# Kernel optimization log

Measured on AMD Instinct MI355X. Metric: run time of the kernel, lower is better.

The kernel has to match this reference:

```python
import jax, jax.numpy as jnp
import numpy as np

N_NODES = 8192
N_EDGES = 65536
D_MODEL = 64
D_INNER = 128
D_STATE = 16
DT_RANK = 4
LAYER_NUM = 3
TAU = 0.01


def _unif(key, shape, fan_out):
    stdv = 1.0 / np.sqrt(fan_out)
    return jax.random.uniform(key, shape, jnp.float32, -stdv, stdv)


def setup_inputs() -> dict:
    key = jax.random.key(0)
    ks = jax.random.split(key, 12)
    x = jax.random.normal(ks[0], (N_NODES, D_MODEL), jnp.float32)
    edge_index = jax.random.randint(ks[1], (2, N_EDGES), 0, N_NODES, jnp.int64)
    in_proj_w = _unif(ks[2], (D_MODEL, 2 * D_INNER), 2 * D_INNER)
    x_proj_w = _unif(ks[3], (D_INNER, DT_RANK + 2 * D_STATE), DT_RANK + 2 * D_STATE)
    dt_proj_w = _unif(ks[4], (DT_RANK, D_INNER), D_INNER)
    out_proj_w = _unif(ks[5], (D_INNER, D_MODEL), D_MODEL)
    A_log = jnp.log(jnp.broadcast_to(jnp.arange(1, D_STATE + 1, dtype=jnp.float32)[None, :], (D_INNER, D_STATE)))
    D = jnp.ones((D_INNER,), jnp.float32)
    in_act_w = _unif(ks[6], (D_INNER, 2), 2)
    in_act_b = _unif(ks[7], (2,), 2)
    out_act_w = _unif(ks[8], (D_INNER, 2), 2)
    out_act_b = _unif(ks[9], (2,), 2)
    return {"x": x, "in_proj_w": in_proj_w, "x_proj_w": x_proj_w, "dt_proj_w": dt_proj_w,
            "A_log": A_log, "D": D, "out_proj_w": out_proj_w,
            "in_act_w": in_act_w, "in_act_b": in_act_b, "out_act_w": out_act_w, "out_act_b": out_act_b,
            "edge_index": edge_index, "layer_num": LAYER_NUM}


def _norm_adj(row, col, w, n_nodes):
    # SparseTensor(...).set_diag() adds diag value 1; symmetric deg^-1/2 renorm
    deg = jax.ops.segment_sum(w, row, num_segments=n_nodes) + 1.0
    dinv = jnp.where(deg > 0, deg ** -0.5, 0.0)
    return dinv[row] * w * dinv[col], dinv * dinv  # off-diag edge weights, diag weights


def _spmm(row, col, ew, dw, x, n_nodes):
    # adj @ x with adj = edges(ew) + diag(dw); x: [N, F]
    return jax.ops.segment_sum(ew[:, None] * x[col], row, num_segments=n_nodes) + dw[:, None] * x


def _gumbel_hard(logits, key, tau):
    g = jax.random.gumbel(key, logits.shape, logits.dtype)
    y = jax.nn.softmax((logits + g) / tau, axis=-1)
    hard = jax.nn.one_hot(jnp.argmax(y, axis=-1), logits.shape[-1], dtype=y.dtype)
    return hard + y - jax.lax.stop_gradient(y)


def reference(x, in_proj_w, x_proj_w, dt_proj_w, A_log, D, out_proj_w,
              in_act_w, in_act_b, out_act_w, out_act_b, edge_index, layer_num):
    n_nodes, d_model = x.shape
    d_inner = dt_proj_w.shape[1]
    n = A_log.shape[1]
    dt_rank = dt_proj_w.shape[0]
    row, col = edge_index[0], edge_index[1]

    xl = jnp.broadcast_to(x[:, None, :], (n_nodes, layer_num, d_model))  # [N,L,d_model]
    x_and_res = xl @ in_proj_w                                           # [N,L,2*d_inner]
    xs, res = jnp.split(x_and_res, 2, axis=-1)
    xs = jax.nn.relu(xs)                                                 # u in scan

    A = -jnp.exp(A_log)                                                  # [d_inner, n]
    x_dbl = xs @ x_proj_w                                                # [N,L,dt_rank+2n]
    delta = jax.nn.softplus(x_dbl[..., :dt_rank] @ dt_proj_w)            # [N,L,d_inner]
    B = x_dbl[..., dt_rank:dt_rank + n]                                  # [N,L,n]
    C = x_dbl[..., dt_rank + n:]                                         # [N,L,n]

    deltaA = jnp.exp(jnp.einsum('bld,dn->bldn', delta, A))               # [N,L,d_inner,n]
    deltaB_u = jnp.einsum('bld,bln->bldn', delta * xs, B)                # [N,L,d_inner,n]

    # initial adjacency: unit-weight edges, sym-normalized with self loops
    ew, dw = _norm_adj(row, col, jnp.ones((row.shape[0],), xs.dtype), n_nodes)
    state = jnp.zeros((n_nodes, d_inner, n), xs.dtype)
    gkey = jax.random.key(42)
    ys = []
    for i in range(layer_num):  # small fixed number of GCN/SSM steps
        state = deltaA[:, i] * state + deltaB_u[:, i]
        y = jnp.einsum('bdn,bn->bd', state, C[:, i])                     # [N,d_inner]
        flat = _spmm(row, col, ew, dw, state.reshape(n_nodes, d_inner * n), n_nodes)
        state = flat.reshape(n_nodes, d_inner, n)
        in_p = _gumbel_hard(y @ in_act_w + in_act_b, jax.random.fold_in(gkey, 2 * i), TAU)
        out_p = _gumbel_hard(y @ out_act_w + out_act_b, jax.random.fold_in(gkey, 2 * i + 1), TAU)
        w = in_p[col, 0] * out_p[row, 0]  # keep_in_prob[v] * keep_out_prob[u]
        ew, dw = _norm_adj(row, col, w, n_nodes)
        ys.append(y)

    y = jnp.stack(ys, axis=1) + xs * D                                   # [N,L,d_inner]
    y = y * jax.nn.relu(res)
    out = y @ out_proj_w                                                 # [N,L,d_model]
    return out[:, -1, :]
```

## Files before the change

### kernel.cpp

```cpp
#include <hip/hip_runtime.h>
#include <cstdint>

#define NN 8192
#define NE 65536
#define G 8
#define CAP 64

typedef _Float16 h8 __attribute__((ext_vector_type(8)));
typedef _Float16 h2 __attribute__((ext_vector_type(2)));

__host__ __device__ inline void tf2x32(uint32_t k0, uint32_t k1,
                                       uint32_t x0, uint32_t x1,
                                       uint32_t& r0, uint32_t& r1) {
  uint32_t ks2 = k0 ^ k1 ^ 0x1BD11BDAu;
  x0 += k0; x1 += k1;
#define TF_ROT(x,d) (((x)<<(d))|((x)>>(32-(d))))
#define TF_R4(ra,rb,rc,rd) \
  x0+=x1; x1=TF_ROT(x1,ra); x1^=x0; \
  x0+=x1; x1=TF_ROT(x1,rb); x1^=x0; \
  x0+=x1; x1=TF_ROT(x1,rc); x1^=x0; \
  x0+=x1; x1=TF_ROT(x1,rd); x1^=x0;
  TF_R4(13,15,26,6)  x0+=k1;  x1+=ks2+1u;
  TF_R4(17,29,16,24) x0+=ks2; x1+=k0+2u;
  TF_R4(13,15,26,6)  x0+=k0;  x1+=k1+3u;
  TF_R4(17,29,16,24) x0+=k1;  x1+=ks2+4u;
  TF_R4(13,15,26,6)  x0+=ks2; x1+=k0+5u;
  r0=x0; r1=x1;
#undef TF_R4
#undef TF_ROT
}

__device__ inline float gumbel32(uint32_t k0, uint32_t k1, uint32_t idx) {
  uint32_t a, b;
  tf2x32(k0, k1, 0u, idx, a, b);
  uint32_t bits = a ^ b;
  float f = __uint_as_float((bits >> 9) | 0x3f800000u) - 1.0f;
  float u = (f > 0.0f) ? f : 1.17549435e-38f;
  return -logf(-logf(u));
}

__global__ void k_scatter(const int* __restrict__ ei, int* __restrict__ cnt,
                          int* __restrict__ csr_col) {
  int e = blockIdx.x*blockDim.x + threadIdx.x;
  if (e < NE) {
    int v = ei[e];
    int pos = atomicAdd(&cnt[v], 1);
    if (pos < CAP) csr_col[(v<<6) + pos] = ei[NE + e];
  }
}

__global__ __launch_bounds__(256) void k_nodeprep(
    const float* __restrict__ x, const float* __restrict__ ipw,
    const float* __restrict__ xpw, const float* __restrict__ dtw,
    const float* __restrict__ iaw, const float* __restrict__ iab,
    const float* __restrict__ oaw, const float* __restrict__ oab,
    const float* __restrict__ alog,
    uint32_t ki0, uint32_t ki1, uint32_t ko0, uint32_t ko1,
    float* __restrict__ xs, float* __restrict__ rres,
    float* __restrict__ delta, _Float16* __restrict__ dxh2,
    float* __restrict__ Bm, _Float16* __restrict__ Bh,
    float* __restrict__ Cm,
    float* __restrict__ inp, float* __restrict__ outp,
    float* __restrict__ Amat) {
  __shared__ float sx[G][64];
  __shared__ float sxs[G][128];
  __shared__ float sdbl[G][36];
  __shared__ float sdx[G][128];
  int t = threadIdx.x;
  int b0 = blockIdx.x * G;
  if (blockIdx.x == 0) {
    for (int i = t; i < 2048; i += 256) Amat[i] = -expf(alog[i]);
  }
  for (int i = t; i < G*64; i += 256) sx[i>>6][i&63] = x[b0*64 + i];
  __syncthreads();
  float acc[G];
#pragma unroll
  for (int g = 0; g < G; g++) acc[g] = 0.f;
  for (int k = 0; k < 64; k++) {
    float w = ipw[k*256 + t];
#pragma unroll
    for (int g = 0; g < G; g++) acc[g] += sx[g][k] * w;
  }
  if (t < 128) {
#pragma unroll
    for (int g = 0; g < G; g++) {
      float v = fmaxf(acc[g], 0.f);
      sxs[g][t] = v;
      xs[(size_t)(b0+g)*128 + t] = v;
    }
  } else {
    int j = t - 128;
#pragma unroll
    for (int g = 0; g < G; g++) rres[(size_t)(b0+g)*128 + j] = fmaxf(acc[g], 0.f);
  }
  __syncthreads();
  for (int idx = t; idx < G*36; idx += 256) {
    int g = idx / 36, c = idx % 36;
    float a = 0.f;
    for (int d = 0; d < 128; d++) a += sxs[g][d] * xpw[d*36 + c];
    sdbl[g][c] = a;
    if (c >= 4 && c < 20) {
      Bm[(b0+g)*16 + (c-4)] = a;
      Bh[(b0+g)*16 + (c-4)] = (_Float16)a;
    } else if (c >= 20)    Cm[(b0+g)*16 + (c-20)] = a;
  }
  __syncthreads();
  {
    int d = t & 127, hi = t >> 7;
#pragma unroll
    for (int gg = 0; gg < G/2; gg++) {
      int g = hi*(G/2) + gg;
      int b = b0 + g;
      float dt = sdbl[g][0]*dtw[d]     + sdbl[g][1]*dtw[128+d]
               + sdbl[g][2]*dtw[256+d] + sdbl[g][3]*dtw[384+d];
      float dv = fmaxf(dt, 0.f) + log1pf(expf(-fabsf(dt)));
      delta[(size_t)b*128 + d] = dv;
      sdx[g][d] = dv * sxs[g][d];
    }
  }
  __syncthreads();
  for (int i = t; i < G*64; i += 256) {
    int g = i >> 6, d = i & 63;
    h2 pk;
    pk.x = (_Float16)sdx[g][d];
    pk.y = (_Float16)sdx[g][d + 64];
    ((h2*)(dxh2 + ((size_t)(b0+g) << 7)))[d] = pk;
  }
  int wid = t >> 6, lane = t & 63;
#pragma unroll
  for (int s = 0; s < 2; s++) {
    int g = wid*2 + s;
    int b = b0 + g;
    float da = sdx[g][lane], db = sdx[g][lane + 64];
    float4 pr;
    pr.x = da*iaw[2*lane]   + db*iaw[2*(lane+64)];
    pr.y = da*iaw[2*lane+1] + db*iaw[2*(lane+64)+1];
    pr.z = da*oaw[2*lane]   + db*oaw[2*(lane+64)];
    pr.w = da*oaw[2*lane+1] + db*oaw[2*(lane+64)+1];
    for (int off = 32; off >= 1; off >>= 1) {
      pr.x += __shfl_down(pr.x, off);
      pr.y += __shfl_down(pr.y, off);
      pr.z += __shfl_down(pr.z, off);
      pr.w += __shfl_down(pr.w, off);
    }
    if (lane == 0) {
      float BC = 0.f;
      for (int n = 0; n < 16; n++) BC += sdbl[g][4+n] * sdbl[g][20+n];
      float li0 = BC*pr.x + iab[0], li1 = BC*pr.y + iab[1];
      float lo0 = BC*pr.z + oab[0], lo1 = BC*pr.w + oab[1];
      uint32_t L0 = 2u*(uint32_t)b, L1 = L0 + 1u;
      inp[b]  = (li0 + gumbel32(ki0, ki1, L0) >= li1 + gumbel32(ki0, ki1, L1)) ? 1.0f : 0.0f;
      outp[b] = (lo0 + gumbel32(ko0, ko1, L0) >= lo1 + gumbel32(ko0, ko1, L1)) ? 1.0f : 0.0f;
    }
  }
}

__global__ __launch_bounds__(256) void k_spmm0f(
    const int* __restrict__ cnt, const int* __restrict__ csr_col,
    const float* __restrict__ inp, const float* __restrict__ outp,
    const float* __restrict__ delta, const _Float16* __restrict__ dxh2,
    const float* __restrict__ Bm, const _Float16* __restrict__ Bh,
    const float* __restrict__ Cm, const float* __restrict__ Amat,
    _Float16* __restrict__ s_out, float* __restrict__ dinv1,
    float* __restrict__ y2p) {
  __shared__ int   sc[2][CAP];
  __shared__ float scoef[2][CAP];
  __shared__ float sdegs[2];
  int t = threadIdx.x, half = t >> 7, tid2 = t & 127;
  int v = (blockIdx.x << 1) + half;
  int deg = min(cnt[v], CAP);
  if (tid2 < 64) {
    float g = 0.f;
    if (tid2 < deg) {
      int c = csr_col[(v<<6) + tid2];
      sc[half][tid2] = c;
      scoef[half][tid2] = 1.0f / sqrtf((float)min(cnt[c], CAP) + 1.0f);
      g = inp[c];
    }
    for (int off = 32; off >= 1; off >>= 1) g += __shfl_down(g, off);
    if (tid2 == 0) sdegs[half] = g;
  }
  __syncthreads();
  int d0 = tid2 >> 1, d1 = d0 + 64, nq = tid2 & 1;
  float dv = 1.0f / sqrtf((float)deg + 1.0f);
  const float4* BmV = (const float4*)(Bm + ((size_t)v << 4));
  float4 Bv0 = BmV[nq*2], Bv1 = BmV[nq*2+1];
  h2 pkv = ((const h2*)(dxh2 + ((size_t)v << 7)))[d0];
  float dx0 = (float)pkv.x, dx1 = (float)pkv.y;
  float dw = dv * dv;
  float c0 = dw * dx0, c1 = dw * dx1;
  float4 a0l = {c0*Bv0.x, c0*Bv0.y, c0*Bv0.z, c0*Bv0.w};
  float4 a0h = {c0*Bv1.x, c0*Bv1.y, c0*Bv1.z, c0*Bv1.w};
  float4 a1l = {c1*Bv0.x, c1*Bv0.y, c1*Bv0.z, c1*Bv0.w};
  float4 a1h = {c1*Bv1.x, c1*Bv1.y, c1*Bv1.z, c1*Bv1.w};
  for (int j = 0; j < deg; j++) {
    int c = sc[half][j];
    float coef = dv * scoef[half][j];
    h2 pk = ((const h2*)(dxh2 + ((size_t)c << 7)))[d0];
    h8 Bp = ((const h8*)(Bh + ((size_t)c << 4)))[nq];
    float e0 = coef * (float)pk.x;
    float e1 = coef * (float)pk.y;
    float b0f = (float)Bp[0], b1f = (float)Bp[1], b2f = (float)Bp[2], b3f = (float)Bp[3];
    float b4f = (float)Bp[4], b5f = (float)Bp[5], b6f = (float)Bp[6], b7f = (float)Bp[7];
    a0l.x += e0*b0f; a0l.y += e0*b1f; a0l.z += e0*b2f; a0l.w += e0*b3f;
    a0h.x += e0*b4f; a0h.y += e0*b5f; a0h.z += e0*b6f; a0h.w += e0*b7f;
    a1l.x += e1*b0f; a1l.y += e1*b1f; a1l.z += e1*b2f; a1l.w += e1*b3f;
    a1h.x += e1*b4f; a1h.y += e1*b5f; a1h.z += e1*b6f; a1h.w += e1*b7f;
  }
  float de0 = delta[v*128 + d0], de1 = delta[v*128 + d1];
  const float4* A0p = (const float4*)(Amat + (d0 << 4));
  const float4* A1p = (const float4*)(Amat + (d1 << 4));
  float4 A00 = A0p[nq*2], A01 = A0p[nq*2+1];
  float4 A10 = A1p[nq*2], A11 = A1p[nq*2+1];
  float4 E0l, E0h, E1l, E1h;
  E0l.x = expf(de0*A00.x); E0l.y = expf(de0*A00.y); E0l.z = expf(de0*A00.z); E0l.w = expf(de0*A00.w);
  E0h.x = expf(de0*A01.x); E0h.y = expf(de0*A01.y); E0h.z = expf(de0*A01.z); E0h.w = expf(de0*A01.w);
  E1l.x = expf(de1*A10.x); E1l.y = expf(de1*A10.y); E1l.z = expf(de1*A10.z); E1l.w = expf(de1*A10.w);
  E1h.x = expf(de1*A11.x); E1h.y = expf(de1*A11.y); E1h.z = expf(de1*A11.z); E1h.w = expf(de1*A11.w);
  float4 s0l, s0h, s1l, s1h;
  s0l.x = E0l.x*a0l.x + dx0*Bv0.x; s0l.y = E0l.y*a0l.y + dx0*Bv0.y;
  s0l.z = E0l.z*a0l.z + dx0*Bv0.z; s0l.w = E0l.w*a0l.w + dx0*Bv0.w;
  s0h.x = E0h.x*a0h.x + dx0*Bv1.x; s0h.y = E0h.y*a0h.y + dx0*Bv1.y;
  s0h.z = E0h.z*a0h.z + dx0*Bv1.z; s0h.w = E0h.w*a0h.w + dx0*Bv1.w;
  s1l.x = E1l.x*a1l.x + dx1*Bv0.x; s1l.y = E1l.y*a1l.y + dx1*Bv0.y;
  s1l.z = E1l.z*a1l.z + dx1*Bv0.z; s1l.w = E1l.w*a1l.w + dx1*Bv0.w;
  s1h.x = E1h.x*a1h.x + dx1*Bv1.x; s1h.y = E1h.y*a1h.y + dx1*Bv1.y;
  s1h.z = E1h.z*a1h.z + dx1*Bv1.z; s1h.w = E1h.w*a1h.w + dx1*Bv1.w;
  if (inp[v] != 0.f) {
    h8* op = (h8*)(s_out + ((size_t)v << 11));
    h8 p0, p1;
    p0[0]=(_Float16)s0l.x; p0[1]=(_Float16)s0l.y; p0[2]=(_Float16)s0l.z; p0[3]=(_Float16)s0l.w;
    p0[4]=(_Float16)s0h.x; p0[5]=(_Float16)s0h.y; p0[6]=(_Float16)s0h.z; p0[7]=(_Float16)s0h.w;
    p1[0]=(_Float16)s1l.x; p1[1]=(_Float16)s1l.y; p1[2]=(_Float16)s1l.z; p1[3]=(_Float16)s1l.w;
    p1[4]=(_Float16)s1h.x; p1[5]=(_Float16)s1h.y; p1[6]=(_Float16)s1h.z; p1[7]=(_Float16)s1h.w;
    op[d0*2 + nq] = p0;
    op[d0*2 + 128 + nq] = p1;
  }
  float degs = sdegs[half];
  float d1v = 1.0f / sqrtf(outp[v]*degs + 1.0f);
  if (tid2 == 0) dinv1[v] = d1v;
  float dw1 = d1v * d1v;
  const float4* CmV = (const float4*)(Cm + ((size_t)v << 4));
  float4 Cv0 = CmV[nq*2], Cv1 = CmV[nq*2+1];
  float BvC = Bv0.x*Cv0.x + Bv0.y*Cv0.y + Bv0.z*Cv0.z + Bv0.w*Cv0.w
            + Bv1.x*Cv1.x + Bv1.y*Cv1.y + Bv1.z*Cv1.z + Bv1.w*Cv1.w;
  float y0p = dw1*(E0l.x*s0l.x*Cv0.x + E0l.y*s0l.y*Cv0.y + E0l.z*s0l.z*Cv0.z + E0l.w*s0l.w*Cv0.w
                 + E0h.x*s0h.x*Cv1.x + E0h.y*s0h.y*Cv1.y + E0h.z*s0h.z*Cv1.z + E0h.w*s0h.w*Cv1.w)
            + dx0*BvC;
  float y1p = dw1*(E1l.x*s1l.x*Cv0.x + E1l.y*s1l.y*Cv0.y + E1l.z*s1l.z*Cv0.z + E1l.w*s1l.w*Cv0.w
                 + E1h.x*s1h.x*Cv1.x + E1h.y*s1h.y*Cv1.y + E1h.z*s1h.z*Cv1.z + E1h.w*s1h.w*Cv1.w)
            + dx1*BvC;
  y0p += __shfl_xor(y0p, 1);
  y1p += __shfl_xor(y1p, 1);
  if (nq == 0) {
    y2p[v*128 + d0] = y0p;
    y2p[v*128 + d1] = y1p;
  }
}

__global__ __launch_bounds__(256) void k_spmm1fo(
    const int* __restrict__ cnt, const int* __restrict__ csr_col,
    const float* __restrict__ dinv1,
    const float* __restrict__ inp, const float* __restrict__ outp,
    const float* __restrict__ delta,
    const float* __restrict__ Cm, const float* __restrict__ Amat,
    const _Float16* __restrict__ s_in, const float* __restrict__ y2p,
    const float* __restrict__ xs, const float* __restrict__ rres,
    const float* __restrict__ Dv, const float* __restrict__ wout,
    float* __restrict__ out) {
  __shared__ int   sc[2][CAP];
  __shared__ float scoef[2][CAP];
  __shared__ int   snact[2];
  __shared__ float ty[2][128];
  __shared__ float sproj[2][64];
  int t = threadIdx.x, half = t >> 7, tid2 = t & 127;
  int v = (blockIdx.x << 1) + half;
  if (tid2 == 0) snact[half] = 0;
  if (tid2 < 64) {
    int deg = (outp[v] != 0.f) ? min(cnt[v], CAP) : 0;
    if (tid2 < deg) {
      int c = csr_col[(v<<6) + tid2];
      if (inp[c] != 0.f) {
        int p = atomicAdd(&snact[half], 1);
        sc[half][p] = c; scoef[half][p] = dinv1[c];
      }
    }
  }
  __syncthreads();
  int nact = snact[half];
  int d0 = tid2 >> 1, d1 = d0 + 64, nq = tid2 & 1;
  float dv = dinv1[v];
  float4 a0l = {0.f,0.f,0.f,0.f}, a0h = {0.f,0.f,0.f,0.f};
  float4 a1l = {0.f,0.f,0.f,0.f}, a1h = {0.f,0.f,0.f,0.f};
  for (int j = 0; j < nact; j++) {
    int c = sc[half][j];
    float coef = dv * scoef[half][j];
    const h8* rp = (const h8*)(s_in + ((size_t)c << 11));
    h8 n0 = rp[d0*2 + nq], n1 = rp[d0*2 + 128 + nq];
    a0l.x += coef*(float)n0[0]; a0l.y += coef*(float)n0[1];
    a0l.z += coef*(float)n0[2]; a0l.w += coef*(float)n0[3];
    a0h.x += coef*(float)n0[4]; a0h.y += coef*(float)n0[5];
    a0h.z += coef*(float)n0[6]; a0h.w += coef*(float)n0[7];
    a1l.x += coef*(float)n1[0]; a1l.y += coef*(float)n1[1];
    a1l.z += coef*(float)n1[2]; a1l.w += coef*(float)n1[3];
    a1h.x += coef*(float)n1[4]; a1h.y += coef*(float)n1[5];
    a1h.z += coef*(float)n1[6]; a1h.w += coef*(float)n1[7];
  }
  float y0g = 0.f, y1g = 0.f;
  if (nact > 0) {
    float de0 = delta[v*128 + d0], de1 = delta[v*128 + d1];
    const float4* A0p = (const float4*)(Amat + (d0 << 4));
    const float4* A1p = (const float4*)(Amat + (d1 << 4));
    float4 A00 = A0p[nq*2], A01 = A0p[nq*2+1];
    float4 A10 = A1p[nq*2], A11 = A1p[nq*2+1];
    const float4* CmV = (const float4*)(Cm + ((size_t)v << 4));
    float4 Cv0 = CmV[nq*2], Cv1 = CmV[nq*2+1];
    y0g = expf(de0*A00.x)*a0l.x*Cv0.x + expf(de0*A00.y)*a0l.y*Cv0.y
        + expf(de0*A00.z)*a0l.z*Cv0.z + expf(de0*A00.w)*a0l.w*Cv0.w
        + expf(de0*A01.x)*a0h.x*Cv1.x + expf(de0*A01.y)*a0h.y*Cv1.y
        + expf(de0*A01.z)*a0h.z*Cv1.z + expf(de0*A01.w)*a0h.w*Cv1.w;
    y1g = expf(de1*A10.x)*a1l.x*Cv0.x + expf(de1*A10.y)*a1l.y*Cv0.y
        + expf(de1*A10.z)*a1l.z*Cv0.z + expf(de1*A10.w)*a1l.w*Cv0.w
        + expf(de1*A11.x)*a1h.x*Cv1.x + expf(de1*A11.y)*a1h.y*Cv1.y
        + expf(de1*A11.z)*a1h.z*Cv1.z + expf(de1*A11.w)*a1h.w*Cv1.w;
  }
  y0g += __shfl_xor(y0g, 1);
  y1g += __shfl_xor(y1g, 1);
  if (nq == 0) {
    float yA = y0g + y2p[v*128 + d0];
    float yB = y1g + y2p[v*128 + d1];
    ty[half][d0] = (yA + xs[v*128 + d0]*Dv[d0]) * rres[v*128 + d0];
    ty[half][d1] = (yB + xs[v*128 + d1]*Dv[d1]) * rres[v*128 + d1];
  }
  __syncthreads();
  int oc = tid2 & 63, ks = tid2 >> 6;
  const float* typ = ty[half];
  float acc = 0.f;
  for (int d = ks*64; d < ks*64 + 64; d++) acc += typ[d] * wout[d*64 + oc];
  if (ks == 1) sproj[half][oc] = acc;
  __syncthreads();
  if (ks == 0) out[v*64 + oc] = acc + sproj[half][oc];
}

extern "C" void kernel_launch(void* const* d_in, const int* in_sizes, int n_in,
                              void* d_out, int out_size, void* d_ws, size_t ws_size,
                              hipStream_t stream) {
  const float* x    = (const float*)d_in[0];
  const float* ipw  = (const float*)d_in[1];
  const float* xpw  = (const float*)d_in[2];
  const float* dtw  = (const float*)d_in[3];
  const float* alog = (const float*)d_in[4];
  const float* Dv   = (const float*)d_in[5];
  const float* wout = (const float*)d_in[6];
  const float* iaw  = (const float*)d_in[7];
  const float* iab  = (const float*)d_in[8];
  const float* oaw  = (const float*)d_in[9];
  const float* oab  = (const float*)d_in[10];
  const int*   ei   = (const int*)d_in[11];
  (void)in_sizes; (void)n_in; (void)out_size; (void)ws_size;

  float* W = (float*)d_ws;
  size_t o = 0;
  float* xs    = W + o; o += (size_t)NN*128;
  float* rres  = W + o; o += (size_t)NN*128;
  float* delta = W + o; o += (size_t)NN*128;
  float* y2p   = W + o; o += (size_t)NN*128;
  float* Bm    = W + o; o += (size_t)NN*16;
  float* Cm    = W + o; o += (size_t)NN*16;
  float* Amat  = W + o; o += 2048;
  float* dinv1 = W + o; o += NN;
  float* inp   = W + o; o += NN;
  float* outp  = W + o; o += NN;
  _Float16* dxh2 = (_Float16*)(W + o); o += (size_t)NN*64;
  _Float16* Bh   = (_Float16*)(W + o); o += (size_t)NN*8;
  _Float16* stA  = (_Float16*)(W + o); o += (size_t)NN*1024;
  int* cnt     = (int*)(W + o);
  int* csr_col = cnt + NN;

  uint32_t ki0, ki1, ko0, ko1;
  tf2x32(0u, 42u, 0u, 0u, ki0, ki1);
  tf2x32(0u, 42u, 0u, 1u, ko0, ko1);

  hipMemsetAsync(cnt, 0, NN*sizeof(int), stream);
  k_scatter<<<NE/256, 256, 0, stream>>>(ei, cnt, csr_col);

  k_nodeprep<<<NN/G, 256, 0, stream>>>(x, ipw, xpw, dtw, iaw, iab, oaw, oab,
                                       alog, ki0, ki1, ko0, ko1,
                                       xs, rres, delta, dxh2, Bm, Bh, Cm,
                                       inp, outp, Amat);

  k_spmm0f<<<NN/2, 256, 0, stream>>>(cnt, csr_col, inp, outp,
                                     delta, dxh2, Bm, Bh, Cm, Amat,
                                     stA, dinv1, y2p);

  k_spmm1fo<<<NN/2, 256, 0, stream>>>(cnt, csr_col, dinv1, inp, outp,
                                      delta, Cm, Amat, stA, y2p,
                                      xs, rres, Dv, wout, (float*)d_out);
}
```

Baseline: 168.8 us.

## Fuse edge scatter into nodeprep, stage fp16 out_proj in LDS, unroll gathers

Removes the separate CSR scatter kernel and folds the edge bucketing into k_nodeprep, where 64 threads per block handle one edge each (1024 blocks cover the 65536 edges). That kernel also converts out_proj weights to fp16. The final kernel copies those weights into 16KB of shared memory per block, so the output projection reads LDS instead of global memory. The neighbor-gather loops in both spmm kernels are unrolled by 4. This saves a launch and global weight reads, but costs fp16 precision in the output projection and per-block LDS copying that may lower occupancy.

```diff
diff --git a/kernel.cpp b/kernel.cpp
--- a/kernel.cpp
+++ b/kernel.cpp
@@ -39,35 +39,37 @@
   return -logf(-logf(u));
 }
 
-__global__ void k_scatter(const int* __restrict__ ei, int* __restrict__ cnt,
-                          int* __restrict__ csr_col) {
-  int e = blockIdx.x*blockDim.x + threadIdx.x;
-  if (e < NE) {
-    int v = ei[e];
-    int pos = atomicAdd(&cnt[v], 1);
-    if (pos < CAP) csr_col[(v<<6) + pos] = ei[NE + e];
-  }
-}
-
 __global__ __launch_bounds__(256) void k_nodeprep(
     const float* __restrict__ x, const float* __restrict__ ipw,
     const float* __restrict__ xpw, const float* __restrict__ dtw,
     const float* __restrict__ iaw, const float* __restrict__ iab,
     const float* __restrict__ oaw, const float* __restrict__ oab,
-    const float* __restrict__ alog,
+    const float* __restrict__ alog, const float* __restrict__ wout,
+    const int* __restrict__ ei,
     uint32_t ki0, uint32_t ki1, uint32_t ko0, uint32_t ko1,
     float* __restrict__ xs, float* __restrict__ rres,
     float* __restrict__ delta, _Float16* __restrict__ dxh2,
     float* __restrict__ Bm, _Float16* __restrict__ Bh,
     float* __restrict__ Cm,
     float* __restrict__ inp, float* __restrict__ outp,
-    float* __restrict__ Amat) {
+    float* __restrict__ Amat, _Float16* __restrict__ woh,
+    int* __restrict__ cnt, int* __restrict__ csr_col) {
   __shared__ float sx[G][64];
   __shared__ float sxs[G][128];
   __shared__ float sdbl[G][36];
   __shared__ float sdx[G][128];
   int t = threadIdx.x;
   int b0 = blockIdx.x * G;
+  if (t < 64) {
+    int e = blockIdx.x * 64 + t;
+    int v = ei[e];
+    int pos = atomicAdd(&cnt[v], 1);
+    if (pos < CAP) csr_col[(v<<6) + pos] = ei[NE + e];
+  }
+  {
+    int i = blockIdx.x * 8 + (t & 7);
+    if (t < 8) woh[i] = (_Float16)wout[i];
+  }
   if (blockIdx.x == 0) {
     for (int i = t; i < 2048; i += 256) Amat[i] = -expf(alog[i]);
   }
@@ -193,6 +195,7 @@
   float4 a0h = {c0*Bv1.x, c0*Bv1.y, c0*Bv1.z, c0*Bv1.w};
   float4 a1l = {c1*Bv0.x, c1*Bv0.y, c1*Bv0.z, c1*Bv0.w};
   float4 a1h = {c1*Bv1.x, c1*Bv1.y, c1*Bv1.z, c1*Bv1.w};
+#pragma unroll 4
   for (int j = 0; j < deg; j++) {
     int c = sc[half][j];
     float coef = dv * scoef[half][j];
@@ -266,15 +269,21 @@
     const float* __restrict__ Cm, const float* __restrict__ Amat,
     const _Float16* __restrict__ s_in, const float* __restrict__ y2p,
     const float* __restrict__ xs, const float* __restrict__ rres,
-    const float* __restrict__ Dv, const float* __restrict__ wout,
+    const float* __restrict__ Dv, const _Float16* __restrict__ woh,
     float* __restrict__ out) {
   __shared__ int   sc[2][CAP];
   __shared__ float scoef[2][CAP];
   __shared__ int   snact[2];
   __shared__ float ty[2][128];
   __shared__ float sproj[2][64];
+  __shared__ _Float16 swout[8192];
   int t = threadIdx.x, half = t >> 7, tid2 = t & 127;
   int v = (blockIdx.x << 1) + half;
+  {
+    const uint4* src = (const uint4*)woh;
+    uint4* dst = (uint4*)swout;
+    for (int i = t; i < 1024; i += 256) dst[i] = src[i];
+  }
   if (tid2 == 0) snact[half] = 0;
   if (tid2 < 64) {
     int deg = (outp[v] != 0.f) ? min(cnt[v], CAP) : 0;
@@ -292,6 +301,7 @@
   float dv = dinv1[v];
   float4 a0l = {0.f,0.f,0.f,0.f}, a0h = {0.f,0.f,0.f,0.f};
   float4 a1l = {0.f,0.f,0.f,0.f}, a1h = {0.f,0.f,0.f,0.f};
+#pragma unroll 4
   for (int j = 0; j < nact; j++) {
     int c = sc[half][j];
     float coef = dv * scoef[half][j];
@@ -336,7 +346,7 @@
   int oc = tid2 & 63, ks = tid2 >> 6;
   const float* typ = ty[half];
   float acc = 0.f;
-  for (int d = ks*64; d < ks*64 + 64; d++) acc += typ[d] * wout[d*64 + oc];
+  for (int d = ks*64; d < ks*64 + 64; d++) acc += typ[d] * (float)swout[d*64 + oc];
   if (ks == 1) sproj[half][oc] = acc;
   __syncthreads();
   if (ks == 0) out[v*64 + oc] = acc + sproj[half][oc];
@@ -373,6 +383,7 @@
   float* outp  = W + o; o += NN;
   _Float16* dxh2 = (_Float16*)(W + o); o += (size_t)NN*64;
   _Float16* Bh   = (_Float16*)(W + o); o += (size_t)NN*8;
+  _Float16* woh  = (_Float16*)(W + o); o += 4096;
   _Float16* stA  = (_Float16*)(W + o); o += (size_t)NN*1024;
   int* cnt     = (int*)(W + o);
   int* csr_col = cnt + NN;
@@ -382,12 +393,11 @@
   tf2x32(0u, 42u, 0u, 1u, ko0, ko1);
 
   hipMemsetAsync(cnt, 0, NN*sizeof(int), stream);
-  k_scatter<<<NE/256, 256, 0, stream>>>(ei, cnt, csr_col);
 
   k_nodeprep<<<NN/G, 256, 0, stream>>>(x, ipw, xpw, dtw, iaw, iab, oaw, oab,
-                                       alog, ki0, ki1, ko0, ko1,
+                                       alog, wout, ei, ki0, ki1, ko0, ko1,
                                        xs, rres, delta, dxh2, Bm, Bh, Cm,
-                                       inp, outp, Amat);
+                                       inp, outp, Amat, woh, cnt, csr_col);
 
   k_spmm0f<<<NN/2, 256, 0, stream>>>(cnt, csr_col, inp, outp,
                                      delta, dxh2, Bm, Bh, Cm, Amat,
@@ -395,5 +405,5 @@
 
   k_spmm1fo<<<NN/2, 256, 0, stream>>>(cnt, csr_col, dinv1, inp, outp,
                                       delta, Cm, Amat, stA, y2p,
-                                      xs, rres, Dv, wout, (float*)d_out);
-}
+                                      xs, rres, Dv, woh, (float*)d_out);
+}
```

After: 168.1 us. About the same (-0.4%).
